# Kernel optimization log

Hardware: AMD Instinct MI355X
Metric: run time of the kernel (lower is better)

The kernel has to match this reference:

```python
import jax, jax.numpy as jnp
import numpy as np

N_NODES = 100000
N_EDGES = 1_600_000
F_IN, HID, N_CLS = 128, 64, 32
NEG_SLOPE = 0.2  # PyG GATv2Conv default


def _segment_softmax(scores, seg, num_segments):
    # numerically stable softmax over edges grouped by destination node
    m = jax.ops.segment_max(scores, seg, num_segments=num_segments)
    ex = jnp.exp(scores - m[seg])
    s = jax.ops.segment_sum(ex, seg, num_segments=num_segments)
    return ex / (s[seg] + 1e-16)


def _gatv2_layer(x, src, dst, Wl, bl, Wr, br, att, bias, num_nodes):
    xl = x @ Wl + bl              # source transform  [N, C]
    xr = x @ Wr + br              # target transform  [N, C]
    # per-edge GATv2 attention logit: a . leaky_relu(xl_j + xr_i)
    e = jax.nn.leaky_relu(xl[src] + xr[dst], NEG_SLOPE) @ att  # [E]
    alpha = _segment_softmax(e, dst, num_nodes)                 # [E]
    out = jax.ops.segment_sum(alpha[:, None] * xl[src], dst, num_segments=num_nodes)
    return out + bias


def _add_self_loops(edge_index, n):
    loops = jnp.arange(n, dtype=edge_index.dtype)
    return jnp.concatenate([edge_index, jnp.stack([loops, loops])], axis=1)


def setup_inputs() -> dict:
    key = jax.random.key(0)
    ks = jax.random.split(key, 8)
    s1 = 1.0 / np.sqrt(F_IN)
    s2 = 1.0 / np.sqrt(HID)
    return {
        "x": jax.random.normal(ks[0], (N_NODES, F_IN), jnp.float32),
        "edge_index": jax.random.randint(ks[1], (2, N_EDGES), 0, N_NODES, jnp.int64),
        "W1l": jax.random.normal(ks[2], (F_IN, HID), jnp.float32) * s1,
        "b1l": jnp.zeros((HID,), jnp.float32),
        "W1r": jax.random.normal(ks[3], (F_IN, HID), jnp.float32) * s1,
        "b1r": jnp.zeros((HID,), jnp.float32),
        "att1": jax.random.normal(ks[4], (HID,), jnp.float32) * s2,
        "bias1": jnp.zeros((HID,), jnp.float32),
        "W2l": jax.random.normal(ks[5], (HID, N_CLS), jnp.float32) * s2,
        "b2l": jnp.zeros((N_CLS,), jnp.float32),
        "W2r": jax.random.normal(ks[6], (HID, N_CLS), jnp.float32) * s2,
        "b2r": jnp.zeros((N_CLS,), jnp.float32),
        "att2": jax.random.normal(ks[7], (N_CLS,), jnp.float32) / np.sqrt(N_CLS),
        "bias2": jnp.zeros((N_CLS,), jnp.float32),
    }


def reference(x, edge_index, W1l, b1l, W1r, b1r, att1, bias1,
              W2l, b2l, W2r, b2r, att2, bias2):
    n = x.shape[0]
    ei = _add_self_loops(edge_index, n)
    src, dst = ei[0], ei[1]
    h = jax.nn.relu(_gatv2_layer(x, src, dst, W1l, b1l, W1r, b1r, att1, bias1, n))
    # F.dropout(training=False) is identity in eval mode
    out = _gatv2_layer(h, src, dst, W2l, b2l, W2r, b2r, att2, bias2, n)
    return out
```

## Files before the change

kernel.cpp:

```cpp
#include <hip/hip_runtime.h>
#include <math.h>

#define F_IN 128
#define HID 64
#define NCLS 32
#define NEG 0.2f
#define NBKT 256
#define CHUNK 8192

__device__ __forceinline__ void f4fma(float4& a, float s, const float4& w) {
    a.x = fmaf(s, w.x, a.x);
    a.y = fmaf(s, w.y, a.y);
    a.z = fmaf(s, w.z, a.z);
    a.w = fmaf(s, w.w, a.w);
}
__device__ __forceinline__ unsigned short f2bf(float f) {
    unsigned u = __float_as_uint(f);
    return (unsigned short)((u + 0x7FFFu + ((u >> 16) & 1u)) >> 16);
}


__global__ __launch_bounds__(256) void zeroBuckets(int* __restrict__ bucketSize, int BK) {
    int i = blockIdx.x * 256 + threadIdx.x;
    if (i < BK) bucketSize[i] = 0;
}

__global__ __launch_bounds__(256) void bucketHist(const int* __restrict__ ei,
                                                  int Eorig, int Etot,
                                                  int* __restrict__ bucketSize, int BK) {
    __shared__ int h[512];
    int t = threadIdx.x;
    for (int j = t; j < BK; j += 256) h[j] = 0;
    __syncthreads();
    int base = blockIdx.x * CHUNK;
    int end = base + CHUNK < Etot ? base + CHUNK : Etot;
    for (int i = base + t; i < end; i += 256) {
        int dst = i < Eorig ? ei[Eorig + i] : i - Eorig;
        atomicAdd(&h[dst >> 8], 1);
    }
    __syncthreads();
    for (int j = t; j < BK; j += 256)
        if (h[j]) atomicAdd(&bucketSize[j], h[j]);
}

__global__ __launch_bounds__(256) void bucketScan(const int* __restrict__ bucketSize,
                                                  int* __restrict__ bucketStart,
                                                  int* __restrict__ bucketCursor,
                                                  int BK, int Etot) {
    __shared__ int sd[256];
    int t = threadIdx.x;
    int v0 = (2 * t     < BK) ? bucketSize[2 * t]     : 0;
    int v1 = (2 * t + 1 < BK) ? bucketSize[2 * t + 1] : 0;
    int ts = v0 + v1;
    sd[t] = ts;
    __syncthreads();
    for (int off = 1; off < 256; off <<= 1) {
        int x = (t >= off) ? sd[t - off] : 0;
        __syncthreads();
        sd[t] += x;
        __syncthreads();
    }
    int excl = sd[t] - ts;
    if (2 * t < BK)     { bucketStart[2 * t] = excl;          bucketCursor[2 * t] = excl; }
    if (2 * t + 1 < BK) { bucketStart[2 * t + 1] = excl + v0; bucketCursor[2 * t + 1] = excl + v0; }
    if (t == 255) bucketStart[BK] = Etot;
}

__global__ __launch_bounds__(256) void bucketScatter(const int* __restrict__ ei,
                                                     int Eorig, int Etot,
                                                     int* __restrict__ bucketCursor,
                                                     int2* __restrict__ pairs, int BK) {
    __shared__ int h[512], lbase[512], hcur[512];
    int t = threadIdx.x;
    for (int j = t; j < BK; j += 256) { h[j] = 0; hcur[j] = 0; }
    __syncthreads();
    int base = blockIdx.x * CHUNK;
    int end = base + CHUNK < Etot ? base + CHUNK : Etot;
    for (int i = base + t; i < end; i += 256) {
        int dst = i < Eorig ? ei[Eorig + i] : i - Eorig;
        atomicAdd(&h[dst >> 8], 1);
    }
    __syncthreads();
    for (int j = t; j < BK; j += 256)
        lbase[j] = h[j] ? atomicAdd(&bucketCursor[j], h[j]) : 0;
    __syncthreads();
    for (int i = base + t; i < end; i += 256) {
        int src, dst;
        if (i < Eorig) { src = ei[i]; dst = ei[Eorig + i]; }
        else           { src = dst = i - Eorig; }
        int b = dst >> 8;
        int off = atomicAdd(&hcur[b], 1);
        pairs[lbase[b] + off] = make_int2(src, dst);
    }
}

__global__ __launch_bounds__(256) void bucketCSR(const int2* __restrict__ pairs,
                                                 const int* __restrict__ bucketStart,
                                                 int* __restrict__ rowstart,
                                                 int* __restrict__ cnt,
                                                 int* __restrict__ srclist, int N) {
    __shared__ int c[256], cur[256];
    int t = threadIdx.x;
    int b = blockIdx.x;
    int lo = b * NBKT;
    int eb = bucketStart[b], ee = bucketStart[b + 1];
    c[t] = 0;
    __syncthreads();
    for (int i = eb + t; i < ee; i += 256)
        atomicAdd(&c[pairs[i].y - lo], 1);
    __syncthreads();
    cur[t] = c[t];
    __syncthreads();
    for (int off = 1; off < 256; off <<= 1) {
        int x = (t >= off) ? cur[t - off] : 0;
        __syncthreads();
        cur[t] += x;
        __syncthreads();
    }
    int excl = cur[t] - c[t];
    int node = lo + t;
    if (node < N) { rowstart[node] = eb + excl; cnt[node] = c[t]; }
    __syncthreads();
    cur[t] = excl;
    __syncthreads();
    for (int i = eb + t; i < ee; i += 256) {
        int2 pr = pairs[i];
        int pos = atomicAdd(&cur[pr.y - lo], 1);
        srclist[eb + pos] = pr.x;
    }
}

__global__ __launch_bounds__(256) void transform1(const float* __restrict__ x,
                                                  const float* __restrict__ Wl,
                                                  const float* __restrict__ bl,
                                                  const float* __restrict__ Wr,
                                                  const float* __restrict__ br,
                                                  unsigned short* __restrict__ xlb,
                                                  float* __restrict__ xr, int N) {
    __shared__ float sWl[64 * HID];
    __shared__ float sWr[64 * HID];
    __shared__ float sx[64][68];
    int t = threadIdx.x;
    int nb = blockIdx.x * 64;
    int c4 = (t & 15) * 4;
    int slot = t >> 4;
    int maxnode = N - nb;

    float4 bl4 = *(const float4*)(bl + c4);
    float4 br4 = *(const float4*)(br + c4);
    float4 accl[4] = {bl4, bl4, bl4, bl4};
    float4 accr[4] = {br4, br4, br4, br4};

    for (int kt = 0; kt < 2; kt++) {
        if (kt) __syncthreads();
#pragma unroll
        for (int j = 0; j < 4; j++) {
            int f = t + j * 256;
            ((float4*)sWl)[f] = ((const float4*)Wl)[kt * 1024 + f];
            ((float4*)sWr)[f] = ((const float4*)Wr)[kt * 1024 + f];
            int node = f >> 4, kc = f & 15;
            float4 v = {0.f, 0.f, 0.f, 0.f};
            if (node < maxnode)
                v = ((const float4*)x)[(size_t)(nb + node) * 32 + kt * 16 + kc];
            *(float4*)&sx[node][kc * 4] = v;
        }
        __syncthreads();

#pragma unroll 4
        for (int k4 = 0; k4 < 16; k4++) {
            int k = k4 * 4;
            float4 wl0 = *(const float4*)&sWl[(k + 0) * HID + c4];
            float4 wl1 = *(const float4*)&sWl[(k + 1) * HID + c4];
            float4 wl2 = *(const float4*)&sWl[(k + 2) * HID + c4];
            float4 wl3 = *(const float4*)&sWl[(k + 3) * HID + c4];
            float4 wr0 = *(const float4*)&sWr[(k + 0) * HID + c4];
            float4 wr1 = *(const float4*)&sWr[(k + 1) * HID + c4];
            float4 wr2 = *(const float4*)&sWr[(k + 2) * HID + c4];
            float4 wr3 = *(const float4*)&sWr[(k + 3) * HID + c4];
#pragma unroll
            for (int j = 0; j < 4; j++) {
                float4 xv = *(const float4*)&sx[slot + j * 16][k];
                f4fma(accl[j], xv.x, wl0); f4fma(accr[j], xv.x, wr0);
                f4fma(accl[j], xv.y, wl1); f4fma(accr[j], xv.y, wr1);
                f4fma(accl[j], xv.z, wl2); f4fma(accr[j], xv.z, wr2);
                f4fma(accl[j], xv.w, wl3); f4fma(accr[j], xv.w, wr3);
            }
        }
    }
#pragma unroll
    for (int j = 0; j < 4; j++) {
        int g = nb + slot + j * 16;
        if (g < N) {
            ushort4 o;
            o.x = f2bf(accl[j].x); o.y = f2bf(accl[j].y);
            o.z = f2bf(accl[j].z); o.w = f2bf(accl[j].w);
            *(ushort4*)(xlb + (size_t)g * HID + c4) = o;
            *(float4*)(xr + (size_t)g * HID + c4) = accr[j];
        }
    }
}

__global__ __launch_bounds__(256) void transform2(const float* __restrict__ h,
                                                  const float* __restrict__ Wl,
                                                  const float* __restrict__ bl,
                                                  const float* __restrict__ Wr,
                                                  const float* __restrict__ br,
                                                  unsigned short* __restrict__ xlb,
                                                  float* __restrict__ xr, int N) {
    __shared__ float sWl[HID * NCLS];
    __shared__ float sWr[HID * NCLS];
    __shared__ float sx[128][68];
    int t = threadIdx.x;
    int nb = blockIdx.x * 128;

#pragma unroll
    for (int j = 0; j < 2; j++) {
        int f = t + j * 256;
        ((float4*)sWl)[f] = ((const float4*)Wl)[f];
        ((float4*)sWr)[f] = ((const float4*)Wr)[f];
    }
    int maxf = (N - nb) * 16;
#pragma unroll
    for (int j = 0; j < 8; j++) {
        int f = t + j * 256;
        int node = f >> 4, kc = f & 15;
        float4 v = {0.f, 0.f, 0.f, 0.f};
        if (f < maxf) v = ((const float4*)(h + (size_t)nb * HID))[f];
        v.x = fmaxf(v.x, 0.f);
        v.y = fmaxf(v.y, 0.f);
        v.z = fmaxf(v.z, 0.f);
        v.w = fmaxf(v.w, 0.f);
        *(float4*)&sx[node][kc * 4] = v;
    }
    __syncthreads();

    int c4 = (t & 7) * 4;
    int slot = t >> 3;
    float4 bl4 = *(const float4*)(bl + c4);
    float4 br4 = *(const float4*)(br + c4);
    float4 accl[4] = {bl4, bl4, bl4, bl4};
    float4 accr[4] = {br4, br4, br4, br4};

#pragma unroll 4
    for (int k4 = 0; k4 < HID / 4; k4++) {
        int k = k4 * 4;
        float4 wl0 = *(const float4*)&sWl[(k + 0) * NCLS + c4];
        float4 wl1 = *(const float4*)&sWl[(k + 1) * NCLS + c4];
        float4 wl2 = *(const float4*)&sWl[(k + 2) * NCLS + c4];
        float4 wl3 = *(const float4*)&sWl[(k + 3) * NCLS + c4];
        float4 wr0 = *(const float4*)&sWr[(k + 0) * NCLS + c4];
        float4 wr1 = *(const float4*)&sWr[(k + 1) * NCLS + c4];
        float4 wr2 = *(const float4*)&sWr[(k + 2) * NCLS + c4];
        float4 wr3 = *(const float4*)&sWr[(k + 3) * NCLS + c4];
#pragma unroll
        for (int j = 0; j < 4; j++) {
            float4 xv = *(const float4*)&sx[slot + j * 32][k];
            f4fma(accl[j], xv.x, wl0); f4fma(accr[j], xv.x, wr0);
            f4fma(accl[j], xv.y, wl1); f4fma(accr[j], xv.y, wr1);
            f4fma(accl[j], xv.z, wl2); f4fma(accr[j], xv.z, wr2);
            f4fma(accl[j], xv.w, wl3); f4fma(accr[j], xv.w, wr3);
        }
    }
#pragma unroll
    for (int j = 0; j < 4; j++) {
        int g = nb + slot + j * 32;
        if (g < N) {
            ushort4 o;
            o.x = f2bf(accl[j].x); o.y = f2bf(accl[j].y);
            o.z = f2bf(accl[j].z); o.w = f2bf(accl[j].w);
            *(ushort4*)(xlb + (size_t)g * NCLS + c4) = o;
            *(float4*)(xr + (size_t)g * NCLS + c4) = accr[j];
        }
    }
}

template <int C>
__global__ __launch_bounds__(256) void fusedAggB(const unsigned short* __restrict__ xlb,
                                                 const float* __restrict__ xr,
                                                 const float* __restrict__ att,
                                                 const int* __restrict__ rowstart,
                                                 const int* __restrict__ cnt,
                                                 const int* __restrict__ srclist,
                                                 const float* __restrict__ bias,
                                                 float* __restrict__ out, int N) {
    const int LPQ = C / 8;
    const int SLOTS = 64 / LPQ;
    int wid = threadIdx.x >> 6;
    int lane = threadIdx.x & 63;
    int n = blockIdx.x * 4 + wid;
    if (n >= N) return;

    int slot = lane / LPQ;
    int pos = lane % LPQ;
    int c8 = pos * 8;

    float xr8[8], at8[8];
    *(float4*)&xr8[0] = *(const float4*)(xr + (size_t)n * C + c8);
    *(float4*)&xr8[4] = *(const float4*)(xr + (size_t)n * C + c8 + 4);
    *(float4*)&at8[0] = *(const float4*)(att + c8);
    *(float4*)&at8[4] = *(const float4*)(att + c8 + 4);

    int row = rowstart[n];
    int deg = cnt[n];

    float s = 0.f;
    float acc[8] = {0.f, 0.f, 0.f, 0.f, 0.f, 0.f, 0.f, 0.f};

    for (int cb = 0; cb < deg; cb += 64) {
        int len = deg - cb; if (len > 64) len = 64;
        int li = lane < len ? lane : len - 1;
        int srcreg = srclist[row + cb + li];
        int nbatch = (len + SLOTS - 1) / SLOTS;
#pragma unroll 2
        for (int b = 0; b < nbatch; b++) {
            int eidx = b * SLOTS + slot;
            int src = __shfl(srcreg, eidx, 64);
            uint4 q = *(const uint4*)(xlb + (size_t)src * C + c8);
            float v[8];
            v[0] = __uint_as_float(q.x << 16);
            v[1] = __uint_as_float(q.x & 0xffff0000u);
            v[2] = __uint_as_float(q.y << 16);
            v[3] = __uint_as_float(q.y & 0xffff0000u);
            v[4] = __uint_as_float(q.z << 16);
            v[5] = __uint_as_float(q.z & 0xffff0000u);
            v[6] = __uint_as_float(q.w << 16);
            v[7] = __uint_as_float(q.w & 0xffff0000u);
            float p = 0.f;
#pragma unroll
            for (int c = 0; c < 8; c++) {
                float u = v[c] + xr8[c];
                u = fmaxf(u, NEG * u);
                p = fmaf(u, at8[c], p);
            }
#pragma unroll
            for (int o = 1; o < LPQ; o <<= 1) p += __shfl_xor(p, o, 64);
            float w = (eidx < len) ? __expf(p) : 0.f;
            s += w;
#pragma unroll
            for (int c = 0; c < 8; c++) acc[c] = fmaf(w, v[c], acc[c]);
        }
    }
#pragma unroll
    for (int o = LPQ; o < 64; o <<= 1) {
#pragma unroll
        for (int c = 0; c < 8; c++) acc[c] += __shfl_xor(acc[c], o, 64);
        s += __shfl_xor(s, o, 64);
    }
    if (lane < LPQ) {
        float bi8[8];
        *(float4*)&bi8[0] = *(const float4*)(bias + c8);
        *(float4*)&bi8[4] = *(const float4*)(bias + c8 + 4);
        float inv = 1.f / (s + 1e-16f);
        float o8[8];
#pragma unroll
        for (int c = 0; c < 8; c++) o8[c] = acc[c] * inv + bi8[c];
        *(float4*)(out + (size_t)n * C + c8)     = *(float4*)&o8[0];
        *(float4*)(out + (size_t)n * C + c8 + 4) = *(float4*)&o8[4];
    }
}

extern "C" void kernel_launch(void* const* d_in, const int* in_sizes, int n_in,
                              void* d_out, int out_size, void* d_ws, size_t ws_size,
                              hipStream_t stream) {
    const float* x     = (const float*)d_in[0];
    const int*   ei    = (const int*)d_in[1];
    const float* W1l   = (const float*)d_in[2];
    const float* b1l   = (const float*)d_in[3];
    const float* W1r   = (const float*)d_in[4];
    const float* b1r   = (const float*)d_in[5];
    const float* att1  = (const float*)d_in[6];
    const float* bias1 = (const float*)d_in[7];
    const float* W2l   = (const float*)d_in[8];
    const float* b2l   = (const float*)d_in[9];
    const float* W2r   = (const float*)d_in[10];
    const float* b2r   = (const float*)d_in[11];
    const float* att2  = (const float*)d_in[12];
    const float* bias2 = (const float*)d_in[13];
    float* out = (float*)d_out;

    int N     = in_sizes[0] / F_IN;
    int Eorig = in_sizes[1] / 2;
    int Etot  = Eorig + N;
    int BK    = (N + NBKT - 1) / NBKT;

    char* p = (char*)d_ws;
    auto alloc = [&](size_t bytes) { void* r = (void*)p; p += (bytes + 255) & ~(size_t)255; return r; };
    unsigned short* xl1b = (unsigned short*)alloc((size_t)N * HID * 2);
    float* xr1     = (float*)alloc((size_t)N * HID * 4);
    float* h       = (float*)alloc((size_t)N * HID * 4);
    unsigned short* xl2b = (unsigned short*)alloc((size_t)N * NCLS * 2);
    float* xr2     = (float*)alloc((size_t)N * NCLS * 4);
    int*   cnt     = (int*)alloc((size_t)N * 4);
    int*   rowstart= (int*)alloc((size_t)N * 4);
    int*   srclist = (int*)alloc((size_t)Etot * 4);
    int*   bucketSize   = (int*)alloc(520 * 4);
    int*   bucketStart  = (int*)alloc(520 * 4);
    int*   bucketCursor = (int*)alloc(520 * 4);
    int2*  pairs   = (int2*)xl2b;

    int nChunks = (Etot + CHUNK - 1) / CHUNK;

    zeroBuckets<<<2, 256, 0, stream>>>(bucketSize, BK);
    bucketHist<<<nChunks, 256, 0, stream>>>(ei, Eorig, Etot, bucketSize, BK);
    bucketScan<<<1, 256, 0, stream>>>(bucketSize, bucketStart, bucketCursor, BK, Etot);
    bucketScatter<<<nChunks, 256, 0, stream>>>(ei, Eorig, Etot, bucketCursor, pairs, BK);
    bucketCSR<<<BK, 256, 0, stream>>>(pairs, bucketStart, rowstart, cnt, srclist, N);

    transform1<<<(N + 63) / 64, 256, 0, stream>>>(x, W1l, b1l, W1r, b1r, xl1b, xr1, N);
    fusedAggB<HID><<<(N + 3) / 4, 256, 0, stream>>>(xl1b, xr1, att1, rowstart, cnt,
                                                    srclist, bias1, h, N);

    transform2<<<(N + 127) / 128, 256, 0, stream>>>(h, W2l, b2l, W2r, b2r, xl2b, xr2, N);
    fusedAggB<NCLS><<<(N + 3) / 4, 256, 0, stream>>>(xl2b, xr2, att2, rowstart, cnt,
                                                     srclist, bias2, out, N);
}
```

Before: 352.0 us.

## Use bf16 MFMA for layer-1 transform with pre-packed weight fragments

Replaces the fp32 FMA tiled GEMM in transform1 with bf16 MFMA 16x16x32 instructions. A small new prep kernel converts Wl and Wr into bf16 B-fragments that each block stages in shared memory. Each wave converts its x rows to bf16 A-fragments in registers. This cuts ALU work for the 128->64 projection but lowers the precision of the x and W inputs to bf16 and writes outputs with scattered per-element stores. The aggregation loop unroll is also raised from 2 to 4.

Measured after the change: 319.4 us. -9.2%, faster.

```diff
diff --git a/kernel.cpp b/kernel.cpp
--- a/kernel.cpp
+++ b/kernel.cpp
@@ -7,6 +7,9 @@
 #define NEG 0.2f
 #define NBKT 256
 #define CHUNK 8192
+
+using bf8 = __attribute__((ext_vector_type(8))) short;
+using f4v = __attribute__((ext_vector_type(4))) float;
 
 __device__ __forceinline__ void f4fma(float4& a, float s, const float4& w) {
     a.x = fmaf(s, w.x, a.x);
@@ -130,72 +133,75 @@
     }
 }
 
+__global__ __launch_bounds__(256) void prepW(const float* __restrict__ Wl,
+                                             const float* __restrict__ Wr,
+                                             uint4* __restrict__ wfrag) {
+    int e = blockIdx.x * 256 + threadIdx.x;
+    if (e >= 2048) return;
+    int lane = e & 63;
+    int kt = (e >> 6) & 3;
+    int ct = (e >> 8) & 3;
+    int mat = e >> 10;
+    const float* W = mat ? Wr : Wl;
+    int k0 = kt * 32 + (lane >> 4) * 8;
+    int c = ct * 16 + (lane & 15);
+    unsigned short h[8];
+#pragma unroll
+    for (int j = 0; j < 8; j++) h[j] = f2bf(W[(k0 + j) * HID + c]);
+    wfrag[e] = *(uint4*)h;
+}
+
 __global__ __launch_bounds__(256) void transform1(const float* __restrict__ x,
-                                                  const float* __restrict__ Wl,
+                                                  const uint4* __restrict__ wfrag,
                                                   const float* __restrict__ bl,
-                                                  const float* __restrict__ Wr,
                                                   const float* __restrict__ br,
                                                   unsigned short* __restrict__ xlb,
                                                   float* __restrict__ xr, int N) {
-    __shared__ float sWl[64 * HID];
-    __shared__ float sWr[64 * HID];
-    __shared__ float sx[64][68];
-    int t = threadIdx.x;
-    int nb = blockIdx.x * 64;
-    int c4 = (t & 15) * 4;
-    int slot = t >> 4;
-    int maxnode = N - nb;
-
-    float4 bl4 = *(const float4*)(bl + c4);
-    float4 br4 = *(const float4*)(br + c4);
-    float4 accl[4] = {bl4, bl4, bl4, bl4};
-    float4 accr[4] = {br4, br4, br4, br4};
-
-    for (int kt = 0; kt < 2; kt++) {
-        if (kt) __syncthreads();
-#pragma unroll
-        for (int j = 0; j < 4; j++) {
-            int f = t + j * 256;
-            ((float4*)sWl)[f] = ((const float4*)Wl)[kt * 1024 + f];
-            ((float4*)sWr)[f] = ((const float4*)Wr)[kt * 1024 + f];
-            int node = f >> 4, kc = f & 15;
-            float4 v = {0.f, 0.f, 0.f, 0.f};
-            if (node < maxnode)
-                v = ((const float4*)x)[(size_t)(nb + node) * 32 + kt * 16 + kc];
-            *(float4*)&sx[node][kc * 4] = v;
-        }
-        __syncthreads();
-
-#pragma unroll 4
-        for (int k4 = 0; k4 < 16; k4++) {
-            int k = k4 * 4;
-            float4 wl0 = *(const float4*)&sWl[(k + 0) * HID + c4];
-            float4 wl1 = *(const float4*)&sWl[(k + 1) * HID + c4];
-            float4 wl2 = *(const float4*)&sWl[(k + 2) * HID + c4];
-            float4 wl3 = *(const float4*)&sWl[(k + 3) * HID + c4];
-            float4 wr0 = *(const float4*)&sWr[(k + 0) * HID + c4];
-            float4 wr1 = *(const float4*)&sWr[(k + 1) * HID + c4];
-            float4 wr2 = *(const float4*)&sWr[(k + 2) * HID + c4];
-            float4 wr3 = *(const float4*)&sWr[(k + 3) * HID + c4];
-#pragma unroll
-            for (int j = 0; j < 4; j++) {
-                float4 xv = *(const float4*)&sx[slot + j * 16][k];
-                f4fma(accl[j], xv.x, wl0); f4fma(accr[j], xv.x, wr0);
-                f4fma(accl[j], xv.y, wl1); f4fma(accr[j], xv.y, wr1);
-                f4fma(accl[j], xv.z, wl2); f4fma(accr[j], xv.z, wr2);
-                f4fma(accl[j], xv.w, wl3); f4fma(accr[j], xv.w, wr3);
+    __shared__ uint4 sw[2048];
+    int t = threadIdx.x;
+#pragma unroll
+    for (int j = 0; j < 8; j++) sw[t + j * 256] = wfrag[t + j * 256];
+    __syncthreads();
+
+    int w = t >> 6, lane = t & 63;
+    int nb = blockIdx.x * 64 + w * 16;
+    int m = lane & 15, quad = lane >> 4;
+
+    int arow = nb + m; if (arow >= N) arow = N - 1;
+    const float* xrow = x + (size_t)arow * F_IN + quad * 8;
+    bf8 afr[4];
+#pragma unroll
+    for (int kt = 0; kt < 4; kt++) {
+        float4 lo = *(const float4*)(xrow + kt * 32);
+        float4 hi = *(const float4*)(xrow + kt * 32 + 4);
+        unsigned short hh[8];
+        hh[0] = f2bf(lo.x); hh[1] = f2bf(lo.y); hh[2] = f2bf(lo.z); hh[3] = f2bf(lo.w);
+        hh[4] = f2bf(hi.x); hh[5] = f2bf(hi.y); hh[6] = f2bf(hi.z); hh[7] = f2bf(hi.w);
+        afr[kt] = *(bf8*)hh;
+    }
+
+#pragma unroll
+    for (int mat = 0; mat < 2; mat++) {
+        const float* bias = mat ? br : bl;
+#pragma unroll
+        for (int ct = 0; ct < 4; ct++) {
+            f4v acc = {0.f, 0.f, 0.f, 0.f};
+#pragma unroll
+            for (int kt = 0; kt < 4; kt++) {
+                bf8 bfr = *(bf8*)&sw[((mat * 4 + ct) * 4 + kt) * 64 + lane];
+                acc = __builtin_amdgcn_mfma_f32_16x16x32_bf16(afr[kt], bfr, acc, 0, 0, 0);
             }
-        }
-    }
-#pragma unroll
-    for (int j = 0; j < 4; j++) {
-        int g = nb + slot + j * 16;
-        if (g < N) {
-            ushort4 o;
-            o.x = f2bf(accl[j].x); o.y = f2bf(accl[j].y);
-            o.z = f2bf(accl[j].z); o.w = f2bf(accl[j].w);
-            *(ushort4*)(xlb + (size_t)g * HID + c4) = o;
-            *(float4*)(xr + (size_t)g * HID + c4) = accr[j];
+            int ch = ct * 16 + m;
+            float bv = bias[ch];
+#pragma unroll
+            for (int reg = 0; reg < 4; reg++) {
+                int node = nb + quad * 4 + reg;
+                if (node < N) {
+                    float o = acc[reg] + bv;
+                    if (mat) xr[(size_t)node * HID + ch] = o;
+                    else     xlb[(size_t)node * HID + ch] = f2bf(o);
+                }
+            }
         }
     }
 }
@@ -311,7 +317,7 @@
         int li = lane < len ? lane : len - 1;
         int srcreg = srclist[row + cb + li];
         int nbatch = (len + SLOTS - 1) / SLOTS;
-#pragma unroll 2
+#pragma unroll 4
         for (int b = 0; b < nbatch; b++) {
             int eidx = b * SLOTS + slot;
             int src = __shfl(srcreg, eidx, 64);
@@ -393,6 +399,7 @@
     int*   cnt     = (int*)alloc((size_t)N * 4);
     int*   rowstart= (int*)alloc((size_t)N * 4);
     int*   srclist = (int*)alloc((size_t)Etot * 4);
+    uint4* wfrag   = (uint4*)alloc(2048 * 16);
     int*   bucketSize   = (int*)alloc(520 * 4);
     int*   bucketStart  = (int*)alloc(520 * 4);
     int*   bucketCursor = (int*)alloc(520 * 4);
@@ -406,7 +413,8 @@
     bucketScatter<<<nChunks, 256, 0, stream>>>(ei, Eorig, Etot, bucketCursor, pairs, BK);
     bucketCSR<<<BK, 256, 0, stream>>>(pairs, bucketStart, rowstart, cnt, srclist, N);
 
-    transform1<<<(N + 63) / 64, 256, 0, stream>>>(x, W1l, b1l, W1r, b1r, xl1b, xr1, N);
+    prepW<<<8, 256, 0, stream>>>(W1l, W1r, wfrag);
+    transform1<<<(N + 63) / 64, 256, 0, stream>>>(x, wfrag, b1l, b1r, xl1b, xr1, N);
     fusedAggB<HID><<<(N + 3) / 4, 256, 0, stream>>>(xl1b, xr1, att1, rowstart, cnt,
                                                     srclist, bias1, h, N);
 
```
